# Kernel optimization log

Measured on AMD Instinct MI355X. Metric: run time of the kernel, lower is better.

## Reference

```python
import jax, jax.numpy as jnp
import numpy as np

B, T, DIM = 4, 2048, 256
H, D = 8, 32          # head_num, att_nfths
FFN = 1024
EPS = 1e-5
SLOPE = 0.01          # LeakyReLU default negative slope


def setup_inputs() -> dict:
    key = jax.random.key(0)
    ks = jax.random.split(key, 16)
    s = 0.02
    inp = {
        "x_input": jax.random.normal(ks[0], (B, T, DIM), jnp.float32),
        "x_input_pos": jax.random.normal(ks[1], (B, T, T, H), jnp.float32),
        "padding_matrix": jnp.zeros((B, T, T), jnp.float32),
        "Wq": jax.random.normal(ks[2], (H * D, DIM), jnp.float32) * s,
        "bq": jnp.zeros((H * D,), jnp.float32),
        "Wk": jax.random.normal(ks[3], (H * D, DIM), jnp.float32) * s,
        "bk": jnp.zeros((H * D,), jnp.float32),
        "Wv": jax.random.normal(ks[4], (H * D, DIM), jnp.float32) * s,
        "bv": jnp.zeros((H * D,), jnp.float32),
        "Wo": jax.random.normal(ks[5], (DIM, H * D), jnp.float32) * s,
        "bo": jnp.zeros((DIM,), jnp.float32),
        "W1": jax.random.normal(ks[6], (FFN, DIM), jnp.float32) * s,
        "b1": jnp.zeros((FFN,), jnp.float32),
        "W2": jax.random.normal(ks[7], (DIM, FFN), jnp.float32) * s,
        "b2": jnp.zeros((DIM,), jnp.float32),
        "g1": jnp.ones((DIM,), jnp.float32),
        "be1": jnp.zeros((DIM,), jnp.float32),
        "g2": jnp.ones((DIM,), jnp.float32),
        "be2": jnp.zeros((DIM,), jnp.float32),
    }
    return inp


def _layernorm(x, g, b):
    mu = jnp.mean(x, axis=-1, keepdims=True)
    var = jnp.mean(jnp.square(x - mu), axis=-1, keepdims=True)
    return (x - mu) * jax.lax.rsqrt(var + EPS) * g + b


def reference(x_input, x_input_pos, padding_matrix,
              Wq, bq, Wk, bk, Wv, bv, Wo, bo,
              W1, b1, W2, b2, g1, be1, g2, be2):
    b, t, _ = x_input.shape
    # projections -> (b, t, H, D)
    q = (x_input @ Wq.T + bq).reshape(b, t, H, D)
    k = (x_input @ Wk.T + bk).reshape(b, t, H, D)
    v = (x_input @ Wv.T + bv).reshape(b, t, H, D)
    # scores: (b, H, t, t); note pos bias is added BEFORE the 1/sqrt(D) scaling
    scores = jnp.einsum('bqhd,bkhd->bhqk', q, k)
    scores = (scores + jnp.transpose(x_input_pos, (0, 3, 1, 2))) / np.sqrt(D).astype(np.float32)
    scores = scores + padding_matrix[:, None, :, :]
    att = jax.nn.softmax(scores, axis=-1)
    ctx = jnp.einsum('bhqk,bkhd->bqhd', att, v).reshape(b, t, H * D)
    att_out = ctx @ Wo.T + bo
    x = _layernorm(x_input + att_out, g1, be1)
    h = x @ W1.T + b1
    h = jnp.where(h >= 0, h, SLOPE * h)  # LeakyReLU
    x2 = h @ W2.T + b2
    x = _layernorm(x + x2, g2, be2)
    return x
```

## Files before the change

### kernel.cpp

```cpp
#include <hip/hip_runtime.h>

typedef unsigned short u16;
typedef unsigned int   u32;
typedef float f32x4 __attribute__((ext_vector_type(4)));
typedef u32   u32x4 __attribute__((ext_vector_type(4)));
typedef u16   u16x4 __attribute__((ext_vector_type(4)));
typedef u16   u16x8 __attribute__((ext_vector_type(8)));
typedef __bf16 bf16x8 __attribute__((ext_vector_type(8)));

#define OFF_X    0x0000000ULL
#define OFF_WQ   0x0400000ULL
#define OFF_WO   0x0460000ULL
#define OFF_W1   0x0480000ULL
#define OFF_W2   0x0500000ULL
#define OFF_Q    0x0580000ULL
#define OFF_K    0x0980000ULL
#define OFF_VT   0x0D80000ULL
#define OFF_CTX  0x1180000ULL

__device__ __forceinline__ u16 f2bf(float f){
  u32 u = __float_as_uint(f);
  return (u16)((u + 0x7FFFu + ((u >> 16) & 1u)) >> 16);
}
__device__ __forceinline__ u32 cvt_pk(float lo, float hi){
  u32 r;
  asm volatile("v_cvt_pk_bf16_f32 %0, %1, %2" : "=v"(r) : "v"(lo), "v"(hi));
  return r;
}
__device__ __forceinline__ bf16x8 ld_bf8(const u16* p){
  return *(const bf16x8*)p;
}
__device__ __forceinline__ bf16x8 lds_bf8(const u16* p){
  return *(const bf16x8*)p;
}
__device__ __forceinline__ f32x4 ntld4(const float* p){
  return __builtin_nontemporal_load((const f32x4*)p);
}
__device__ __forceinline__ float ntld(const float* p){
  return __builtin_nontemporal_load(p);
}
__device__ __forceinline__ f32x4 MFMA(bf16x8 a, bf16x8 b, f32x4 c){
  return __builtin_amdgcn_mfma_f32_16x16x32_bf16(a, b, c, 0, 0, 0);
}
__device__ __forceinline__ void lbar(){
  asm volatile("s_waitcnt lgkmcnt(0)" ::: "memory");
  __builtin_amdgcn_s_barrier();
}
template<int C>
__device__ __forceinline__ float dpp_rot(float x){
  int i = __float_as_int(x);
  return __int_as_float(__builtin_amdgcn_update_dpp(i, i, C, 0xF, 0xF, false));
}
__device__ __forceinline__ float rmax16(float x){
  x = fmaxf(x, dpp_rot<0x121>(x)); x = fmaxf(x, dpp_rot<0x122>(x));
  x = fmaxf(x, dpp_rot<0x124>(x)); x = fmaxf(x, dpp_rot<0x128>(x));
  return x;
}
__device__ __forceinline__ float rsum16(float x){
  x += dpp_rot<0x121>(x); x += dpp_rot<0x122>(x);
  x += dpp_rot<0x124>(x); x += dpp_rot<0x128>(x);
  return x;
}

__global__ __launch_bounds__(256) void prep_kernel(
    const float* __restrict__ x,  const float* __restrict__ Wq,
    const float* __restrict__ Wk, const float* __restrict__ Wv,
    const float* __restrict__ Wo, const float* __restrict__ W1,
    const float* __restrict__ W2, u16* __restrict__ dst)
{
  int i = (blockIdx.x * 256 + threadIdx.x) * 4;
  const float* src;
  int off;
  if (i < 2097152){ src = x; off = i; }
  else {
    int j = i - 2097152;
    if      (j <  65536){ src = Wq; off = j; }
    else if (j < 131072){ src = Wk; off = j -  65536; }
    else if (j < 196608){ src = Wv; off = j - 131072; }
    else if (j < 262144){ src = Wo; off = j - 196608; }
    else if (j < 524288){ src = W1; off = j - 262144; }
    else                { src = W2; off = j - 524288; }
  }
  f32x4 v = *(const f32x4*)(src + off);
  u16x4 o;
  o[0] = f2bf(v[0]); o[1] = f2bf(v[1]); o[2] = f2bf(v[2]); o[3] = f2bf(v[3]);
  *(u16x4*)(dst + i) = o;
}

__global__ __launch_bounds__(512) void qkv_kernel(
    const u16* __restrict__ X, const u16* __restrict__ W3,
    const float* __restrict__ bq, const float* __restrict__ bk,
    const float* __restrict__ bv,
    u16* __restrict__ Q, u16* __restrict__ K, u16* __restrict__ VT)
{
  __shared__ u16 vtile[32][264];
  const int tid = threadIdx.x;
  const int lane = tid & 63, w = tid >> 6;
  const int g = lane >> 4, c = lane & 15;
  const int m0 = blockIdx.x * 32;
  const int nb = blockIdx.y;
  const u16* Wb = W3 + nb * 65536;
  const float* bias = (nb == 0) ? bq : ((nb == 1) ? bk : bv);
  const int n0 = w * 32;

  f32x4 acc[2][2];
  #pragma unroll
  for (int i = 0; i < 2; ++i)
    #pragma unroll
    for (int j = 0; j < 2; ++j){ f32x4 z = {0.f,0.f,0.f,0.f}; acc[i][j] = z; }

  #pragma unroll
  for (int kt = 0; kt < 8; ++kt){
    bf16x8 a0 = ld_bf8(X  + (size_t)(m0 +      c) * 256 + kt*32 + g*8);
    bf16x8 a1 = ld_bf8(X  + (size_t)(m0 + 16 + c) * 256 + kt*32 + g*8);
    bf16x8 b0 = ld_bf8(Wb + (size_t)(n0 +      c) * 256 + kt*32 + g*8);
    bf16x8 b1 = ld_bf8(Wb + (size_t)(n0 + 16 + c) * 256 + kt*32 + g*8);
    acc[0][0] = MFMA(a0, b0, acc[0][0]);
    acc[0][1] = MFMA(a0, b1, acc[0][1]);
    acc[1][0] = MFMA(a1, b0, acc[1][0]);
    acc[1][1] = MFMA(a1, b1, acc[1][1]);
  }

  const int bi = m0 >> 11, tbase = m0 & 2047;

  if (nb == 2){
    #pragma unroll
    for (int qt = 0; qt < 2; ++qt)
    #pragma unroll
    for (int nt = 0; nt < 2; ++nt)
    #pragma unroll
    for (int r = 0; r < 4; ++r){
      int row = qt*16 + g*4 + r;
      int col = n0 + nt*16 + c;
      vtile[row][col] = f2bf(acc[qt][nt][r] + bias[col]);
    }
    __syncthreads();
    #pragma unroll
    for (int s = 0; s < 2; ++s){
      int u = tid*2 + s;
      int h = u >> 7, d = (u >> 2) & 31, sl0 = (u & 3) * 8;
      u16x8 o;
      #pragma unroll
      for (int jj = 0; jj < 8; ++jj){
        int sl = sl0 + jj;
        int tt = (sl >> 1) + ((sl & 1) << 4);
        o[jj] = vtile[tt][h*32 + d];
      }
      *(u16x8*)(VT + ((size_t)(bi*8 + h) * 32 + d) * 2048 + tbase + sl0) = o;
    }
  } else {
    #pragma unroll
    for (int qt = 0; qt < 2; ++qt)
    #pragma unroll
    for (int nt = 0; nt < 2; ++nt)
    #pragma unroll
    for (int r = 0; r < 4; ++r){
      int mrow = m0 + qt*16 + g*4 + r;
      int col  = n0 + nt*16 + c;
      float v = acc[qt][nt][r] + bias[col];
      int t = mrow & 2047;
      int h = col >> 5, d = col & 31;
      u16 hv = f2bf(v);
      if (nb == 0) Q[((size_t)(bi*8 + h) * 2048 + t) * 32 + d] = hv;
      else         K[((size_t)(bi*8 + h) * 2048 + t) * 32 + d] = hv;
    }
  }
}

__global__ __launch_bounds__(512, 4) void attn_kernel(
    const float* __restrict__ pos, const float* __restrict__ pad,
    const u16* __restrict__ Q, const u16* __restrict__ K,
    const u16* __restrict__ VT, u16* __restrict__ ctx)
{
  __shared__ u32 bias_lds[2][4608];
  __shared__ u32 p_lds[8][16][34];

  const int tid = threadIdx.x;
  const int lane = tid & 63, w = tid >> 6;
  const int g = lane >> 4, c = lane & 15;
  const int bid = blockIdx.x;
  const int xcd = bid & 7;
  const int b = xcd >> 1;
  const int qtile = ((bid >> 3) << 1) | (xcd & 1);
  const int q0 = qtile * 16;
  const int start = (bid >> 3) & 31;

  const u16* Qb  = Q  + ((size_t)(b*8 + w) * 2048 + q0) * 32;
  const u16* Kb  = K  +  (size_t)(b*8 + w) * 2048 * 32;
  const u16* VTb = VT +  (size_t)(b*8 + w) * 32 * 2048;

  const float c1 = 1.4426950408889634f * 0.17677669529663689f;
  const float c2 = 1.4426950408889634f;

  bf16x8 qf = ld_bf8(Qb + (size_t)c * 32 + g*8);

  f32x4 O[2];
  { f32x4 z = {0.f,0.f,0.f,0.f}; O[0] = z; O[1] = z; }
  float m_[4], l_[4];
  #pragma unroll
  for (int r = 0; r < 4; ++r){ m_[r] = -3.0e38f; l_[r] = 0.f; }

  const int li = (lane >> 1) & 15;
  const int ls = lane >> 5;
  const int h0 = (lane & 1) * 4;

  f32x4 fa[2], fb[2];
  float pa_[2], pb_[2];
  bf16x8 kf[4], knf[4], vf[4];

  auto stage_load = [&](int k0){
    #pragma unroll
    for (int j = 0; j < 2; ++j){
      int qr = w*2 + j;
      int k1 = ls*32 + li;
      const float* pr = pos + ((size_t)(b*2048 + q0 + qr) * 2048 + k0) * 8 + h0;
      fa[j] = ntld4(pr + (size_t)k1 * 8);
      fb[j] = ntld4(pr + (size_t)(k1 + 16) * 8);
      const float* dr = pad + (size_t)(b*2048 + q0 + qr) * 2048 + k0 + k1;
      pa_[j] = ntld(dr);
      pb_[j] = ntld(dr + 16);
    }
  };
  auto stage_write = [&](u32* bl){
    #pragma unroll
    for (int j = 0; j < 2; ++j){
      int qr = w*2 + j;
      float plo = pa_[j] * c2, phi = pb_[j] * c2;
      int base = qr*36 + ls*16 + li;
      #pragma unroll
      for (int j2 = 0; j2 < 4; ++j2){
        float lo = fmaf(fa[j][j2], c1, plo);
        float hi = fmaf(fb[j][j2], c1, phi);
        bl[(h0 + j2)*576 + base] = cvt_pk(lo, hi);
      }
    }
  };
  auto load_k = [&](int k0, bf16x8* kd){
    kd[0] = ld_bf8(Kb + (size_t)(k0 +      c) * 32 + g*8);
    kd[1] = ld_bf8(Kb + (size_t)(k0 + 16 + c) * 32 + g*8);
    kd[2] = ld_bf8(Kb + (size_t)(k0 + 32 + c) * 32 + g*8);
    kd[3] = ld_bf8(Kb + (size_t)(k0 + 48 + c) * 32 + g*8);
  };
  auto load_v = [&](int k0){
    vf[0] = ld_bf8(VTb + (size_t)(     c) * 2048 + k0      + g*8);
    vf[1] = ld_bf8(VTb + (size_t)(16 + c) * 2048 + k0      + g*8);
    vf[2] = ld_bf8(VTb + (size_t)(     c) * 2048 + k0 + 32 + g*8);
    vf[3] = ld_bf8(VTb + (size_t)(16 + c) * 2048 + k0 + 32 + g*8);
  };

  stage_load(start * 64);
  stage_write(&bias_lds[0][0]);
  stage_load(((start + 1) & 31) * 64);
  load_k(start * 64, kf);
  lbar();

  for (int i = 0; i < 32; ++i){
    const int k0 = ((start + i) & 31) * 64;
    load_v(k0);
    if (i < 31) stage_write(&bias_lds[(i + 1) & 1][0]);
    if (i < 30) stage_load(((start + i + 2) & 31) * 64);
    if (i < 31) load_k(((start + i + 1) & 31) * 64, knf);

    __builtin_amdgcn_s_setprio(1);

    f32x4 sS[4];
    {
      f32x4 z = {0.f,0.f,0.f,0.f};
      sS[0] = MFMA(qf, kf[0], z);
      sS[1] = MFMA(qf, kf[1], z);
      sS[2] = MFMA(qf, kf[2], z);
      sS[3] = MFMA(qf, kf[3], z);
    }

    const u32* blc = &bias_lds[i & 1][w*576];
    #pragma unroll
    for (int r = 0; r < 4; ++r){
      int rowb = (g*4 + r)*36;
      u32 dwA = blc[rowb + c];
      u32 dwB = blc[rowb + 16 + c];
      float v0 = fmaf(sS[0][r], c1, __uint_as_float(dwA << 16));
      float v1 = fmaf(sS[1][r], c1, __uint_as_float(dwA & 0xFFFF0000u));
      float v2 = fmaf(sS[2][r], c1, __uint_as_float(dwB << 16));
      float v3 = fmaf(sS[3][r], c1, __uint_as_float(dwB & 0xFFFF0000u));
      float mx = rmax16(fmaxf(fmaxf(v0, v1), fmaxf(v2, v3)));
      float mo = m_[r];
      float mn = fmaxf(mo, mx);
      float alpha = exp2f(mo - mn);
      m_[r] = mn;
      float p0 = exp2f(v0 - mn);
      float p1 = exp2f(v1 - mn);
      float p2 = exp2f(v2 - mn);
      float p3 = exp2f(v3 - mn);
      float ps = rsum16((p0 + p1) + (p2 + p3));
      l_[r] = l_[r] * alpha + ps;
      O[0][r] *= alpha;
      O[1][r] *= alpha;
      p_lds[w][g*4 + r][c]      = cvt_pk(p0, p1);
      p_lds[w][g*4 + r][16 + c] = cvt_pk(p2, p3);
    }

    {
      u32x4 t0 = { p_lds[w][c][g*4 + 0], p_lds[w][c][g*4 + 1],
                   p_lds[w][c][g*4 + 2], p_lds[w][c][g*4 + 3] };
      u32x4 t1 = { p_lds[w][c][16 + g*4 + 0], p_lds[w][c][16 + g*4 + 1],
                   p_lds[w][c][16 + g*4 + 2], p_lds[w][c][16 + g*4 + 3] };
      bf16x8 pa0 = __builtin_bit_cast(bf16x8, t0);
      bf16x8 pa1 = __builtin_bit_cast(bf16x8, t1);
      O[0] = MFMA(pa0, vf[0], O[0]);
      O[1] = MFMA(pa0, vf[1], O[1]);
      O[0] = MFMA(pa1, vf[2], O[0]);
      O[1] = MFMA(pa1, vf[3], O[1]);
    }

    __builtin_amdgcn_s_setprio(0);

    #pragma unroll
    for (int j = 0; j < 4; ++j) kf[j] = knf[j];
    lbar();
  }

  #pragma unroll
  for (int r = 0; r < 4; ++r){
    float inv = 1.0f / l_[r];
    int q = q0 + g*4 + r;
    size_t base = (size_t)(b*2048 + q) * 256 + w*32;
    ctx[base +      c] = f2bf(O[0][r] * inv);
    ctx[base + 16 + c] = f2bf(O[1][r] * inv);
  }
}

__global__ __launch_bounds__(512, 2) void tail_kernel(
    const u16* __restrict__ ctx, const u16* __restrict__ Wo,
    const float* __restrict__ bo, const float* __restrict__ x,
    const float* __restrict__ g1, const float* __restrict__ be1,
    const u16* __restrict__ W1, const float* __restrict__ b1,
    const u16* __restrict__ W2, const float* __restrict__ b2,
    const float* __restrict__ g2, const float* __restrict__ be2,
    float* __restrict__ out)
{
  __shared__ u16 x1t[32*256];
  __shared__ u16 ht[32*512];
  __shared__ float sm1[32][8], sm2[32][8];

  const int tid = threadIdx.x;
  const int lane = tid & 63, w = tid >> 6;
  const int g = lane >> 4, c = lane & 15;
  const int m0 = blockIdx.x * 32;
  const int n0 = w * 32;

  f32x4 acc[2][2];
  #pragma unroll
  for (int i = 0; i < 2; ++i)
    #pragma unroll
    for (int j = 0; j < 2; ++j){ f32x4 z = {0.f,0.f,0.f,0.f}; acc[i][j] = z; }

  #pragma unroll
  for (int kt = 0; kt < 8; ++kt){
    bf16x8 a0 = ld_bf8(ctx + (size_t)(m0 +      c) * 256 + kt*32 + g*8);
    bf16x8 a1 = ld_bf8(ctx + (size_t)(m0 + 16 + c) * 256 + kt*32 + g*8);
    bf16x8 b0 = ld_bf8(Wo  + (size_t)(n0 +      c) * 256 + kt*32 + g*8);
    bf16x8 b1v= ld_bf8(Wo  + (size_t)(n0 + 16 + c) * 256 + kt*32 + g*8);
    acc[0][0] = MFMA(a0, b0, acc[0][0]);
    acc[0][1] = MFMA(a0, b1v, acc[0][1]);
    acc[1][0] = MFMA(a1, b0, acc[1][0]);
    acc[1][1] = MFMA(a1, b1v, acc[1][1]);
  }

  float val[2][2][4];
  #pragma unroll
  for (int qt = 0; qt < 2; ++qt)
  #pragma unroll
  for (int nt = 0; nt < 2; ++nt)
  #pragma unroll
  for (int r = 0; r < 4; ++r){
    int mrow = m0 + qt*16 + g*4 + r;
    int col  = n0 + nt*16 + c;
    val[qt][nt][r] = acc[qt][nt][r] + bo[col] + x[(size_t)mrow*256 + col];
  }

  #pragma unroll
  for (int qt = 0; qt < 2; ++qt)
  #pragma unroll
  for (int r = 0; r < 4; ++r){
    float v0 = val[qt][0][r], v1 = val[qt][1][r];
    float p1 = rsum16(v0 + v1);
    float p2 = rsum16(v0*v0 + v1*v1);
    if (c == 0){
      int rr = qt*16 + g*4 + r;
      sm1[rr][w] = p1; sm2[rr][w] = p2;
    }
  }
  __syncthreads();

  float yv[2][2][4];
  #pragma unroll
  for (int qt = 0; qt < 2; ++qt)
  #pragma unroll
  for (int r = 0; r < 4; ++r){
    int rr = qt*16 + g*4 + r;
    float S1 = 0.f, S2 = 0.f;
    #pragma unroll
    for (int j = 0; j < 8; ++j){ S1 += sm1[rr][j]; S2 += sm2[rr][j]; }
    float mean = S1 * (1.0f/256.0f);
    float var  = S2 * (1.0f/256.0f) - mean*mean;
    float rstd = rsqrtf(var + 1e-5f);
    #pragma unroll
    for (int nt = 0; nt < 2; ++nt){
      int col = n0 + nt*16 + c;
      float y = (val[qt][nt][r] - mean) * rstd * g1[col] + be1[col];
      yv[qt][nt][r] = y;
      int elem = rr*256 + col;
      x1t[elem ^ ((rr & 7) << 3)] = f2bf(y);
    }
  }
  __syncthreads();

  f32x4 acc3[2][2];
  #pragma unroll
  for (int i = 0; i < 2; ++i)
    #pragma unroll
    for (int j = 0; j < 2; ++j){ f32x4 z = {0.f,0.f,0.f,0.f}; acc3[i][j] = z; }

  #pragma unroll
  for (int half = 0; half < 2; ++half){
    #pragma unroll
    for (int ns = 0; ns < 2; ++ns){
      const int ncol = half*512 + w*64 + ns*32;
      f32x4 acc2[2][2];
      #pragma unroll
      for (int i = 0; i < 2; ++i)
        #pragma unroll
        for (int j = 0; j < 2; ++j){ f32x4 z = {0.f,0.f,0.f,0.f}; acc2[i][j] = z; }
      #pragma unroll
      for (int kt = 0; kt < 8; ++kt){
        int e0 = (     c)*256 + kt*32 + g*8;
        int e1 = (16 + c)*256 + kt*32 + g*8;
        bf16x8 a0 = lds_bf8(x1t + (e0 ^ ((c & 7) << 3)));
        bf16x8 a1 = lds_bf8(x1t + (e1 ^ (((16 + c) & 7) << 3)));
        bf16x8 b0 = ld_bf8(W1 + (size_t)(ncol +      c) * 256 + kt*32 + g*8);
        bf16x8 b1v= ld_bf8(W1 + (size_t)(ncol + 16 + c) * 256 + kt*32 + g*8);
        acc2[0][0] = MFMA(a0, b0, acc2[0][0]);
        acc2[0][1] = MFMA(a0, b1v, acc2[0][1]);
        acc2[1][0] = MFMA(a1, b0, acc2[1][0]);
        acc2[1][1] = MFMA(a1, b1v, acc2[1][1]);
      }
      #pragma unroll
      for (int qt = 0; qt < 2; ++qt)
      #pragma unroll
      for (int nt = 0; nt < 2; ++nt)
      #pragma unroll
      for (int r = 0; r < 4; ++r){
        int row = qt*16 + g*4 + r;
        int gcol = ncol + nt*16 + c;
        float v = acc2[qt][nt][r] + b1[gcol];
        v = (v >= 0.f) ? v : v * 0.01f;
        int elem = row*512 + (gcol - half*512);
        ht[elem ^ ((row & 7) << 3)] = f2bf(v);
      }
    }
    __syncthreads();

    #pragma unroll
    for (int kt = 0; kt < 16; ++kt){
      int e0 = (     c)*512 + kt*32 + g*8;
      int e1 = (16 + c)*512 + kt*32 + g*8;
      bf16x8 a0 = lds_bf8(ht + (e0 ^ ((c & 7) << 3)));
      bf16x8 a1 = lds_bf8(ht + (e1 ^ (((16 + c) & 7) << 3)));
      int kg = half*512 + kt*32 + g*8;
      bf16x8 b0 = ld_bf8(W2 + (size_t)(n0 +      c) * 1024 + kg);
      bf16x8 b1v= ld_bf8(W2 + (size_t)(n0 + 16 + c) * 1024 + kg);
      acc3[0][0] = MFMA(a0, b0, acc3[0][0]);
      acc3[0][1] = MFMA(a0, b1v, acc3[0][1]);
      acc3[1][0] = MFMA(a1, b0, acc3[1][0]);
      acc3[1][1] = MFMA(a1, b1v, acc3[1][1]);
    }
    __syncthreads();
  }

  float val3[2][2][4];
  #pragma unroll
  for (int qt = 0; qt < 2; ++qt)
  #pragma unroll
  for (int nt = 0; nt < 2; ++nt)
  #pragma unroll
  for (int r = 0; r < 4; ++r){
    int col = n0 + nt*16 + c;
    val3[qt][nt][r] = acc3[qt][nt][r] + b2[col] + yv[qt][nt][r];
  }

  #pragma unroll
  for (int qt = 0; qt < 2; ++qt)
  #pragma unroll
  for (int r = 0; r < 4; ++r){
    float v0 = val3[qt][0][r], v1 = val3[qt][1][r];
    float p1 = rsum16(v0 + v1);
    float p2 = rsum16(v0*v0 + v1*v1);
    if (c == 0){
      int rr = qt*16 + g*4 + r;
      sm1[rr][w] = p1; sm2[rr][w] = p2;
    }
  }
  __syncthreads();

  #pragma unroll
  for (int qt = 0; qt < 2; ++qt)
  #pragma unroll
  for (int r = 0; r < 4; ++r){
    int rr = qt*16 + g*4 + r;
    float S1 = 0.f, S2 = 0.f;
    #pragma unroll
    for (int j = 0; j < 8; ++j){ S1 += sm1[rr][j]; S2 += sm2[rr][j]; }
    float mean = S1 * (1.0f/256.0f);
    float var  = S2 * (1.0f/256.0f) - mean*mean;
    float rstd = rsqrtf(var + 1e-5f);
    int mrow = m0 + rr;
    #pragma unroll
    for (int nt = 0; nt < 2; ++nt){
      int col = n0 + nt*16 + c;
      out[(size_t)mrow*256 + col] = (val3[qt][nt][r] - mean) * rstd * g2[col] + be2[col];
    }
  }
}

extern "C" void kernel_launch(void* const* d_in, const int* in_sizes, int n_in,
                              void* d_out, int out_size, void* d_ws, size_t ws_size,
                              hipStream_t stream)
{
  (void)in_sizes; (void)n_in; (void)out_size; (void)ws_size;
  const float* x   = (const float*)d_in[0];
  const float* pos = (const float*)d_in[1];
  const float* pad = (const float*)d_in[2];
  const float* Wq  = (const float*)d_in[3];
  const float* bq  = (const float*)d_in[4];
  const float* Wk  = (const float*)d_in[5];
  const float* bk  = (const float*)d_in[6];
  const float* Wv  = (const float*)d_in[7];
  const float* bv  = (const float*)d_in[8];
  const float* Wo  = (const float*)d_in[9];
  const float* bo  = (const float*)d_in[10];
  const float* W1  = (const float*)d_in[11];
  const float* b1  = (const float*)d_in[12];
  const float* W2  = (const float*)d_in[13];
  const float* b2  = (const float*)d_in[14];
  const float* g1  = (const float*)d_in[15];
  const float* be1 = (const float*)d_in[16];
  const float* g2  = (const float*)d_in[17];
  const float* be2 = (const float*)d_in[18];

  char* ws = (char*)d_ws;
  u16* wsX  = (u16*)(ws + OFF_X);
  u16* wsW3 = (u16*)(ws + OFF_WQ);
  u16* wsWo = (u16*)(ws + OFF_WO);
  u16* wsW1 = (u16*)(ws + OFF_W1);
  u16* wsW2 = (u16*)(ws + OFF_W2);
  u16* Qb   = (u16*)(ws + OFF_Q);
  u16* Kb   = (u16*)(ws + OFF_K);
  u16* VTb  = (u16*)(ws + OFF_VT);
  u16* ctx  = (u16*)(ws + OFF_CTX);

  prep_kernel<<<2816, 256, 0, stream>>>(x, Wq, Wk, Wv, Wo, W1, W2, wsX);
  qkv_kernel<<<dim3(256, 3), 512, 0, stream>>>(wsX, wsW3, bq, bk, bv, Qb, Kb, VTb);
  attn_kernel<<<512, 512, 0, stream>>>(pos, pad, Qb, Kb, VTb, ctx);
  tail_kernel<<<256, 512, 0, stream>>>(ctx, wsWo, bo, x, g1, be1,
                                       wsW1, b1, wsW2, b2, g2, be2, (float*)d_out);
}
```

Baseline: 228.1 us.

## Skip online-softmax rescale unless row max grows past threshold; stagger start tiles

The softmax loop now computes all scores and row maxima first, then rescales the running max, sum and output accumulators only when any lane's new max exceeds the old one by more than 8 (in log2 units). This removes per-iteration exp2 and multiply work for alpha on most tiles, at the cost of letting exponentials reach up to 2^8 before renormalisation. The key-tile starting offset is also shifted for the second half of blocks, to spread concurrent blocks across different K/V/bias regions.

```diff
diff --git a/kernel.cpp b/kernel.cpp
--- a/kernel.cpp
+++ b/kernel.cpp
@@ -183,7 +183,7 @@
   const int b = xcd >> 1;
   const int qtile = ((bid >> 3) << 1) | (xcd & 1);
   const int q0 = qtile * 16;
-  const int start = (bid >> 3) & 31;
+  const int start = ((bid >> 3) + ((bid >> 8) << 4)) & 31;
 
   const u16* Qb  = Q  + ((size_t)(b*8 + w) * 2048 + q0) * 32;
   const u16* Kb  = K  +  (size_t)(b*8 + w) * 2048 * 32;
@@ -273,28 +273,40 @@
     }
 
     const u32* blc = &bias_lds[i & 1][w*576];
+    float vv[4][4], mx4[4];
     #pragma unroll
     for (int r = 0; r < 4; ++r){
       int rowb = (g*4 + r)*36;
       u32 dwA = blc[rowb + c];
       u32 dwB = blc[rowb + 16 + c];
-      float v0 = fmaf(sS[0][r], c1, __uint_as_float(dwA << 16));
-      float v1 = fmaf(sS[1][r], c1, __uint_as_float(dwA & 0xFFFF0000u));
-      float v2 = fmaf(sS[2][r], c1, __uint_as_float(dwB << 16));
-      float v3 = fmaf(sS[3][r], c1, __uint_as_float(dwB & 0xFFFF0000u));
-      float mx = rmax16(fmaxf(fmaxf(v0, v1), fmaxf(v2, v3)));
-      float mo = m_[r];
-      float mn = fmaxf(mo, mx);
-      float alpha = exp2f(mo - mn);
-      m_[r] = mn;
-      float p0 = exp2f(v0 - mn);
-      float p1 = exp2f(v1 - mn);
-      float p2 = exp2f(v2 - mn);
-      float p3 = exp2f(v3 - mn);
+      vv[r][0] = fmaf(sS[0][r], c1, __uint_as_float(dwA << 16));
+      vv[r][1] = fmaf(sS[1][r], c1, __uint_as_float(dwA & 0xFFFF0000u));
+      vv[r][2] = fmaf(sS[2][r], c1, __uint_as_float(dwB << 16));
+      vv[r][3] = fmaf(sS[3][r], c1, __uint_as_float(dwB & 0xFFFF0000u));
+      mx4[r] = rmax16(fmaxf(fmaxf(vv[r][0], vv[r][1]), fmaxf(vv[r][2], vv[r][3])));
+    }
+    bool need = false;
+    #pragma unroll
+    for (int r = 0; r < 4; ++r) need = need || (mx4[r] - m_[r] > 8.0f);
+    if (__any(need)){
+      #pragma unroll
+      for (int r = 0; r < 4; ++r){
+        float mn = fmaxf(m_[r], mx4[r]);
+        float alpha = exp2f(m_[r] - mn);
+        m_[r] = mn;
+        l_[r] *= alpha;
+        O[0][r] *= alpha;
+        O[1][r] *= alpha;
+      }
+    }
+    #pragma unroll
+    for (int r = 0; r < 4; ++r){
+      float p0 = exp2f(vv[r][0] - m_[r]);
+      float p1 = exp2f(vv[r][1] - m_[r]);
+      float p2 = exp2f(vv[r][2] - m_[r]);
+      float p3 = exp2f(vv[r][3] - m_[r]);
       float ps = rsum16((p0 + p1) + (p2 + p3));
-      l_[r] = l_[r] * alpha + ps;
-      O[0][r] *= alpha;
-      O[1][r] *= alpha;
+      l_[r] += ps;
       p_lds[w][g*4 + r][c]      = cvt_pk(p0, p1);
       p_lds[w][g*4 + r][16 + c] = cvt_pk(p2, p3);
     }
```

Result: no change. 228.4 us (+0.2%).

## Compute transposed scores to keep softmax probabilities in registers, dropping LDS round-trip

Applied to the files above, without the earlier changes.

The score MFMA now runs with K and Q operands swapped, so each lane holds one query column. The softmax probabilities can then feed the PV product directly as 16x16x16 MFMA B-operands, with no trip through shared memory. V^T is written with a permuted key order to match the register layout. Bias staging and pad loads are re-laid out to fit, and row max/sum use ds_swizzle/bpermute instead of DPP reductions. This removes the p_lds write/read and its bank traffic, but adds cross-lane permutes and uses smaller MFMA shapes.

```diff
diff --git a/kernel.cpp b/kernel.cpp
--- a/kernel.cpp
+++ b/kernel.cpp
@@ -3,7 +3,9 @@
 typedef unsigned short u16;
 typedef unsigned int   u32;
 typedef float f32x4 __attribute__((ext_vector_type(4)));
+typedef float f32x2 __attribute__((ext_vector_type(2)));
 typedef u32   u32x4 __attribute__((ext_vector_type(4)));
+typedef u32   u32x2 __attribute__((ext_vector_type(2)));
 typedef u16   u16x4 __attribute__((ext_vector_type(4)));
 typedef u16   u16x8 __attribute__((ext_vector_type(8)));
 typedef __bf16 bf16x8 __attribute__((ext_vector_type(8)));
@@ -36,25 +38,30 @@
 __device__ __forceinline__ f32x4 ntld4(const float* p){
   return __builtin_nontemporal_load((const f32x4*)p);
 }
-__device__ __forceinline__ float ntld(const float* p){
-  return __builtin_nontemporal_load(p);
+__device__ __forceinline__ f32x2 ntld2(const float* p){
+  return __builtin_nontemporal_load((const f32x2*)p);
 }
 __device__ __forceinline__ f32x4 MFMA(bf16x8 a, bf16x8 b, f32x4 c){
   return __builtin_amdgcn_mfma_f32_16x16x32_bf16(a, b, c, 0, 0, 0);
+}
+__device__ __forceinline__ f32x4 MFMA16(u32x2 a, u32x2 b, f32x4 c){
+  asm("v_mfma_f32_16x16x16_bf16 %0, %1, %2, %0" : "+v"(c) : "v"(a), "v"(b));
+  return c;
 }
 __device__ __forceinline__ void lbar(){
   asm volatile("s_waitcnt lgkmcnt(0)" ::: "memory");
   __builtin_amdgcn_s_barrier();
+}
+__device__ __forceinline__ float xhop16(float x){
+  return __int_as_float(__builtin_amdgcn_ds_swizzle(__float_as_int(x), 0x401F));
+}
+__device__ __forceinline__ float xhop32(int idx32, float x){
+  return __int_as_float(__builtin_amdgcn_ds_bpermute(idx32, __float_as_int(x)));
 }
 template<int C>
 __device__ __forceinline__ float dpp_rot(float x){
   int i = __float_as_int(x);
   return __int_as_float(__builtin_amdgcn_update_dpp(i, i, C, 0xF, 0xF, false));
-}
-__device__ __forceinline__ float rmax16(float x){
-  x = fmaxf(x, dpp_rot<0x121>(x)); x = fmaxf(x, dpp_rot<0x122>(x));
-  x = fmaxf(x, dpp_rot<0x124>(x)); x = fmaxf(x, dpp_rot<0x128>(x));
-  return x;
 }
 __device__ __forceinline__ float rsum16(float x){
   x += dpp_rot<0x121>(x); x += dpp_rot<0x122>(x);
@@ -143,7 +150,7 @@
       #pragma unroll
       for (int jj = 0; jj < 8; ++jj){
         int sl = sl0 + jj;
-        int tt = (sl >> 1) + ((sl & 1) << 4);
+        int tt = ((sl >> 2) & 1) * 16 + (sl >> 3) * 4 + (sl & 3);
         o[jj] = vtile[tt][h*32 + d];
       }
       *(u16x8*)(VT + ((size_t)(bi*8 + h) * 32 + d) * 2048 + tbase + sl0) = o;
@@ -172,8 +179,7 @@
     const u16* __restrict__ Q, const u16* __restrict__ K,
     const u16* __restrict__ VT, u16* __restrict__ ctx)
 {
-  __shared__ u32 bias_lds[2][4608];
-  __shared__ u32 p_lds[8][16][34];
+  __shared__ u32 bias_lds[2][4480];
 
   const int tid = threadIdx.x;
   const int lane = tid & 63, w = tid >> 6;
@@ -184,6 +190,7 @@
   const int qtile = ((bid >> 3) << 1) | (xcd & 1);
   const int q0 = qtile * 16;
   const int start = (bid >> 3) & 31;
+  const int idx32 = (lane ^ 32) << 2;
 
   const u16* Qb  = Q  + ((size_t)(b*8 + w) * 2048 + q0) * 32;
   const u16* Kb  = K  +  (size_t)(b*8 + w) * 2048 * 32;
@@ -194,44 +201,37 @@
 
   bf16x8 qf = ld_bf8(Qb + (size_t)c * 32 + g*8);
 
-  f32x4 O[2];
-  { f32x4 z = {0.f,0.f,0.f,0.f}; O[0] = z; O[1] = z; }
-  float m_[4], l_[4];
-  #pragma unroll
-  for (int r = 0; r < 4; ++r){ m_[r] = -3.0e38f; l_[r] = 0.f; }
-
-  const int li = (lane >> 1) & 15;
-  const int ls = lane >> 5;
-  const int h0 = (lane & 1) * 4;
+  f32x4 O0, O1;
+  { f32x4 z = {0.f,0.f,0.f,0.f}; O0 = z; O1 = z; }
+  float m_ = -3.0e38f, l_ = 0.f;
+
+  const int hq = lane & 1, h0 = hq * 4;
+  const int P  = ((lane >> 1) & 15) | ((lane >> 5) << 4);
 
   f32x4 fa[2], fb[2];
-  float pa_[2], pb_[2];
-  bf16x8 kf[4], knf[4], vf[4];
+  f32x2 pd[2];
+  bf16x8 kf[4], knf[4], vfr[2][2];
 
   auto stage_load = [&](int k0){
+    #pragma unroll
+    for (int j = 0; j < 2; ++j){
+      size_t row = (size_t)(b*2048 + q0 + w*2 + j);
+      const float* pr = pos + (row*2048 + k0 + 2*P)*8 + h0;
+      fa[j] = ntld4(pr);
+      fb[j] = ntld4(pr + 8);
+      pd[j] = ntld2(pad + row*2048 + k0 + 2*P);
+    }
+  };
+  auto stage_write = [&](u32* bl){
     #pragma unroll
     for (int j = 0; j < 2; ++j){
       int qr = w*2 + j;
-      int k1 = ls*32 + li;
-      const float* pr = pos + ((size_t)(b*2048 + q0 + qr) * 2048 + k0) * 8 + h0;
-      fa[j] = ntld4(pr + (size_t)k1 * 8);
-      fb[j] = ntld4(pr + (size_t)(k1 + 16) * 8);
-      const float* dr = pad + (size_t)(b*2048 + q0 + qr) * 2048 + k0 + k1;
-      pa_[j] = ntld(dr);
-      pb_[j] = ntld(dr + 16);
-    }
-  };
-  auto stage_write = [&](u32* bl){
-    #pragma unroll
-    for (int j = 0; j < 2; ++j){
-      int qr = w*2 + j;
-      float plo = pa_[j] * c2, phi = pb_[j] * c2;
-      int base = qr*36 + ls*16 + li;
-      #pragma unroll
-      for (int j2 = 0; j2 < 4; ++j2){
-        float lo = fmaf(fa[j][j2], c1, plo);
-        float hi = fmaf(fb[j][j2], c1, phi);
-        bl[(h0 + j2)*576 + base] = cvt_pk(lo, hi);
+      float plo = pd[j][0] * c2, phi = pd[j][1] * c2;
+      #pragma unroll
+      for (int i2 = 0; i2 < 4; ++i2){
+        float lo = fmaf(fa[j][i2], c1, plo);
+        float hi = fmaf(fb[j][i2], c1, phi);
+        bl[(h0 + i2)*560 + qr*35 + P] = cvt_pk(lo, hi);
       }
     }
   };
@@ -242,10 +242,10 @@
     kd[3] = ld_bf8(Kb + (size_t)(k0 + 48 + c) * 32 + g*8);
   };
   auto load_v = [&](int k0){
-    vf[0] = ld_bf8(VTb + (size_t)(     c) * 2048 + k0      + g*8);
-    vf[1] = ld_bf8(VTb + (size_t)(16 + c) * 2048 + k0      + g*8);
-    vf[2] = ld_bf8(VTb + (size_t)(     c) * 2048 + k0 + 32 + g*8);
-    vf[3] = ld_bf8(VTb + (size_t)(16 + c) * 2048 + k0 + 32 + g*8);
+    vfr[0][0] = ld_bf8(VTb + (size_t)(     c) * 2048 + k0      + g*8);
+    vfr[0][1] = ld_bf8(VTb + (size_t)(16 + c) * 2048 + k0      + g*8);
+    vfr[1][0] = ld_bf8(VTb + (size_t)(     c) * 2048 + k0 + 32 + g*8);
+    vfr[1][1] = ld_bf8(VTb + (size_t)(16 + c) * 2048 + k0 + 32 + g*8);
   };
 
   stage_load(start * 64);
@@ -256,7 +256,6 @@
 
   for (int i = 0; i < 32; ++i){
     const int k0 = ((start + i) & 31) * 64;
-    load_v(k0);
     if (i < 31) stage_write(&bias_lds[(i + 1) & 1][0]);
     if (i < 30) stage_load(((start + i + 2) & 31) * 64);
     if (i < 31) load_k(((start + i + 1) & 31) * 64, knf);
@@ -266,50 +265,68 @@
     f32x4 sS[4];
     {
       f32x4 z = {0.f,0.f,0.f,0.f};
-      sS[0] = MFMA(qf, kf[0], z);
-      sS[1] = MFMA(qf, kf[1], z);
-      sS[2] = MFMA(qf, kf[2], z);
-      sS[3] = MFMA(qf, kf[3], z);
-    }
-
-    const u32* blc = &bias_lds[i & 1][w*576];
-    #pragma unroll
-    for (int r = 0; r < 4; ++r){
-      int rowb = (g*4 + r)*36;
-      u32 dwA = blc[rowb + c];
-      u32 dwB = blc[rowb + 16 + c];
-      float v0 = fmaf(sS[0][r], c1, __uint_as_float(dwA << 16));
-      float v1 = fmaf(sS[1][r], c1, __uint_as_float(dwA & 0xFFFF0000u));
-      float v2 = fmaf(sS[2][r], c1, __uint_as_float(dwB << 16));
-      float v3 = fmaf(sS[3][r], c1, __uint_as_float(dwB & 0xFFFF0000u));
-      float mx = rmax16(fmaxf(fmaxf(v0, v1), fmaxf(v2, v3)));
-      float mo = m_[r];
-      float mn = fmaxf(mo, mx);
-      float alpha = exp2f(mo - mn);
-      m_[r] = mn;
-      float p0 = exp2f(v0 - mn);
-      float p1 = exp2f(v1 - mn);
-      float p2 = exp2f(v2 - mn);
-      float p3 = exp2f(v3 - mn);
-      float ps = rsum16((p0 + p1) + (p2 + p3));
-      l_[r] = l_[r] * alpha + ps;
-      O[0][r] *= alpha;
-      O[1][r] *= alpha;
-      p_lds[w][g*4 + r][c]      = cvt_pk(p0, p1);
-      p_lds[w][g*4 + r][16 + c] = cvt_pk(p2, p3);
-    }
-
-    {
-      u32x4 t0 = { p_lds[w][c][g*4 + 0], p_lds[w][c][g*4 + 1],
-                   p_lds[w][c][g*4 + 2], p_lds[w][c][g*4 + 3] };
-      u32x4 t1 = { p_lds[w][c][16 + g*4 + 0], p_lds[w][c][16 + g*4 + 1],
-                   p_lds[w][c][16 + g*4 + 2], p_lds[w][c][16 + g*4 + 3] };
-      bf16x8 pa0 = __builtin_bit_cast(bf16x8, t0);
-      bf16x8 pa1 = __builtin_bit_cast(bf16x8, t1);
-      O[0] = MFMA(pa0, vf[0], O[0]);
-      O[1] = MFMA(pa0, vf[1], O[1]);
-      O[0] = MFMA(pa1, vf[2], O[0]);
-      O[1] = MFMA(pa1, vf[3], O[1]);
+      sS[0] = MFMA(kf[0], qf, z);
+      sS[1] = MFMA(kf[1], qf, z);
+      sS[2] = MFMA(kf[2], qf, z);
+      sS[3] = MFMA(kf[3], qf, z);
+    }
+    load_v(k0);
+
+    const u32* blc = &bias_lds[i & 1][w*560 + c*35];
+    float vv[4][4];
+    #pragma unroll
+    for (int t = 0; t < 4; ++t){
+      u32 dwA = blc[8*t + 2*g];
+      u32 dwB = blc[8*t + 2*g + 1];
+      vv[t][0] = fmaf(sS[t][0], c1, __uint_as_float(dwA << 16));
+      vv[t][1] = fmaf(sS[t][1], c1, __uint_as_float(dwA & 0xFFFF0000u));
+      vv[t][2] = fmaf(sS[t][2], c1, __uint_as_float(dwB << 16));
+      vv[t][3] = fmaf(sS[t][3], c1, __uint_as_float(dwB & 0xFFFF0000u));
+    }
+
+    float mx = vv[0][0];
+    #pragma unroll
+    for (int t = 0; t < 4; ++t)
+      #pragma unroll
+      for (int r = 0; r < 4; ++r)
+        if (t || r) mx = fmaxf(mx, vv[t][r]);
+    mx = fmaxf(mx, xhop16(mx));
+    mx = fmaxf(mx, xhop32(idx32, mx));
+    float mn = fmaxf(m_, mx);
+    float alpha = exp2f(m_ - mn);
+    m_ = mn;
+
+    u32 pk[4][2];
+    float ps = 0.f;
+    #pragma unroll
+    for (int t = 0; t < 4; ++t){
+      float p0 = exp2f(vv[t][0] - mn);
+      float p1 = exp2f(vv[t][1] - mn);
+      float p2 = exp2f(vv[t][2] - mn);
+      float p3 = exp2f(vv[t][3] - mn);
+      ps += (p0 + p1) + (p2 + p3);
+      pk[t][0] = cvt_pk(p0, p1);
+      pk[t][1] = cvt_pk(p2, p3);
+    }
+    ps += xhop16(ps);
+    ps += xhop32(idx32, ps);
+    l_ = l_ * alpha + ps;
+    O0 *= alpha;
+    O1 *= alpha;
+
+    #pragma unroll
+    for (int h32 = 0; h32 < 2; ++h32){
+      u32x4 va = __builtin_bit_cast(u32x4, vfr[h32][0]);
+      u32x4 vb = __builtin_bit_cast(u32x4, vfr[h32][1]);
+      #pragma unroll
+      for (int t2 = 0; t2 < 2; ++t2){
+        int t = h32*2 + t2;
+        u32x2 a0 = { va[t2*2], va[t2*2 + 1] };
+        u32x2 a1 = { vb[t2*2], vb[t2*2 + 1] };
+        u32x2 bf = { pk[t][0], pk[t][1] };
+        O0 = MFMA16(a0, bf, O0);
+        O1 = MFMA16(a1, bf, O1);
+      }
     }
 
     __builtin_amdgcn_s_setprio(0);
@@ -319,13 +336,21 @@
     lbar();
   }
 
-  #pragma unroll
-  for (int r = 0; r < 4; ++r){
-    float inv = 1.0f / l_[r];
-    int q = q0 + g*4 + r;
-    size_t base = (size_t)(b*2048 + q) * 256 + w*32;
-    ctx[base +      c] = f2bf(O[0][r] * inv);
-    ctx[base + 16 + c] = f2bf(O[1][r] * inv);
+  asm volatile("s_nop 7\n\ts_nop 7");
+
+  float inv = 1.0f / l_;
+  size_t base = (size_t)(b*2048 + q0 + c) * 256 + w*32;
+  {
+    u16x4 o;
+    #pragma unroll
+    for (int r = 0; r < 4; ++r) o[r] = f2bf(O0[r] * inv);
+    *(u16x4*)(ctx + base + g*4) = o;
+  }
+  {
+    u16x4 o;
+    #pragma unroll
+    for (int r = 0; r < 4; ++r) o[r] = f2bf(O1[r] * inv);
+    *(u16x4*)(ctx + base + 16 + g*4) = o;
   }
 }
 
```

Measured after the change: 256.3 us. 12.4% more time.
